# Optimization experiments

Hardware: AMD Instinct MI355X
Metric: run time of the kernel (lower is better)

The kernel has to match this reference:

```python
import jax, jax.numpy as jnp
import numpy as np

DIM = 640
HEADS = 10
HEAD_DIM = DIM // HEADS
SCALE = DIM ** (-0.5)  # note: module scales by full dim**-0.5, not head_dim


def setup_inputs() -> dict:
    key = jax.random.key(0)
    ks = jax.random.split(key, 5)
    B, N = 16, 1024
    x = jax.random.normal(ks[0], (B, N, DIM), dtype=jnp.float32)
    w_qkv = jax.random.normal(ks[1], (DIM, 3 * DIM), dtype=jnp.float32) * (DIM ** -0.5)
    b_qkv = jnp.zeros((3 * DIM,), dtype=jnp.float32)
    w_out = jax.random.normal(ks[2], (DIM, DIM), dtype=jnp.float32) * (DIM ** -0.5)
    b_out = jnp.zeros((DIM,), dtype=jnp.float32)
    return {"x": x, "w_qkv": w_qkv, "b_qkv": b_qkv, "w_out": w_out, "b_out": b_out}


def reference(x, w_qkv, b_qkv, w_out, b_out):
    B, N, _ = x.shape
    qkv = x @ w_qkv + b_qkv                     # [B, N, 3*DIM]
    qkv = qkv.reshape(B, N, 3, HEADS, HEAD_DIM)
    q, k, v = qkv[:, :, 0], qkv[:, :, 1], qkv[:, :, 2]   # [B, N, H, Dh]
    # scores: QK^T scaled by dim**-0.5 (module's normfactor)
    scores = jnp.einsum('bihd,bjhd->bhij', q, k) * SCALE  # [B, H, N, N]
    attn = jax.nn.softmax(scores, axis=-1)
    out = jnp.einsum('bhij,bjhd->bihd', attn, v)          # [B, N, H, Dh]
    out = out.reshape(B, N, DIM)
    return out @ w_out + b_out
```

## Files before the change

### kernel.cpp

```cpp
#include <hip/hip_runtime.h>

#define DIM 640
#define NHEADS 10
#define HDIM 64
#define SEQ 1024
#define BATCH 16
#define MROWS (BATCH * SEQ)
#define QKVN (3 * DIM)
#define NBH (BATCH * NHEADS)

typedef float f32x4 __attribute__((ext_vector_type(4)));
typedef __bf16 bf16x8 __attribute__((ext_vector_type(8)));

#define SM_C 0.057027536f

__device__ __forceinline__ unsigned short f2b(float f) {
  union { __bf16 h; unsigned short u; } v;
  v.h = (__bf16)f;
  return v.u;
}

__device__ __forceinline__ f32x4 mfma16(bf16x8 a, bf16x8 b, f32x4 c) {
  return __builtin_amdgcn_mfma_f32_16x16x32_bf16(a, b, c, 0, 0, 0);
}

typedef __attribute__((address_space(3))) unsigned int as3_u32;
typedef const __attribute__((address_space(1))) unsigned int as1_u32;
__device__ __forceinline__ void glds16(const unsigned short* g, unsigned short* l) {
  __builtin_amdgcn_global_load_lds((as1_u32*)g, (as3_u32*)l, 16, 0, 0);
}

__global__ __launch_bounds__(256) void convert_x(
    const float* __restrict__ X, unsigned short* __restrict__ xb) {
  int i = (blockIdx.x * 256 + threadIdx.x) * 4;
  float4 v = *(const float4*)(X + i);
  ushort4 s;
  s.x = f2b(v.x); s.y = f2b(v.y); s.z = f2b(v.z); s.w = f2b(v.w);
  *(ushort4*)(xb + i) = s;
}

__global__ __launch_bounds__(256) void transpose_w(
    const float* __restrict__ W, unsigned short* __restrict__ Wt, int R, int C) {
  __shared__ int tile[32][33];
  const int tx = threadIdx.x & 31, ty = threadIdx.x >> 5;
  const int c0 = blockIdx.x * 32, r0 = blockIdx.y * 32;
#pragma unroll
  for (int i = 0; i < 4; ++i)
    tile[ty + 8 * i][tx] = f2b(W[(r0 + ty + 8 * i) * C + c0 + tx]);
  __syncthreads();
#pragma unroll
  for (int i = 0; i < 4; ++i)
    Wt[(c0 + ty + 8 * i) * R + r0 + tx] = (unsigned short)tile[tx][ty + 8 * i];
}

__global__ __launch_bounds__(256) void qkv_gemm(
    const unsigned short* __restrict__ A, const unsigned short* __restrict__ Bt,
    const float* __restrict__ bias,
    unsigned short* __restrict__ qw, unsigned short* __restrict__ kw,
    unsigned short* __restrict__ vtw) {
  __shared__ __attribute__((aligned(16))) unsigned short As[128 * 64];
  __shared__ __attribute__((aligned(16))) unsigned short Bs[128 * 64];
  const int t = threadIdx.x;
  const int lane = t & 63, w = t >> 6;
  const int quad = lane >> 4, cl = lane & 15;
  const int m0 = blockIdx.y * 128, n0 = blockIdx.x * 128;
  const int wr = (w >> 1) * 64, wc = (w & 1) * 64;

  const int r8 = lane >> 3;
  const int sw = ((lane & 7) ^ r8) * 8;
  const unsigned short* asrc = A + (size_t)(m0 + w * 32 + r8) * DIM + sw;
  const unsigned short* bsrc = Bt + (size_t)(n0 + w * 32 + r8) * DIM + sw;

  const int x = cl & 7;
  const int aoff0 = (wr + cl) * 64 + (quad ^ x) * 8;
  const int aoff1 = (wr + cl) * 64 + ((4 + quad) ^ x) * 8;
  const int boff0 = (wc + cl) * 64 + (quad ^ x) * 8;
  const int boff1 = (wc + cl) * 64 + ((4 + quad) ^ x) * 8;

  f32x4 acc[4][4];
#pragma unroll
  for (int i = 0; i < 4; ++i)
#pragma unroll
    for (int j = 0; j < 4; ++j) acc[i][j] = (f32x4){0.f, 0.f, 0.f, 0.f};

  for (int kt = 0; kt < DIM / 64; ++kt) {
    __syncthreads();
#pragma unroll
    for (int i = 0; i < 4; ++i) {
      glds16(asrc + (size_t)i * 8 * DIM, &As[(w * 32 + i * 8) * 64]);
      glds16(bsrc + (size_t)i * 8 * DIM, &Bs[(w * 32 + i * 8) * 64]);
    }
    asrc += 64; bsrc += 64;
    __syncthreads();
#pragma unroll
    for (int ks = 0; ks < 2; ++ks) {
      const int ao = ks ? aoff1 : aoff0, bo = ks ? boff1 : boff0;
      bf16x8 af[4], bfr[4];
#pragma unroll
      for (int i = 0; i < 4; ++i) af[i] = *(const bf16x8*)&As[ao + i * 1024];
#pragma unroll
      for (int j = 0; j < 4; ++j) bfr[j] = *(const bf16x8*)&Bs[bo + j * 1024];
#pragma unroll
      for (int i = 0; i < 4; ++i)
#pragma unroll
        for (int j = 0; j < 4; ++j) acc[i][j] = mfma16(af[i], bfr[j], acc[i][j]);
    }
  }

  const int sec = n0 / DIM;
  unsigned short* qk = (sec == 0) ? qw : kw;
  const float sc = (sec == 0) ? SM_C : 1.0f;
#pragma unroll
  for (int j = 0; j < 4; ++j) {
    int cc = n0 + wc + j * 16 + cl;
    int cr = cc - sec * DIM;
    int h = cr >> 6, d = cr & 63;
    float bv = bias[cc];
#pragma unroll
    for (int i = 0; i < 4; ++i) {
      int rbase = m0 + wr + i * 16 + quad * 4;
      int b = rbase >> 10, n = rbase & 1023;
      int bh = b * NHEADS + h;
      if (sec < 2) {
        size_t base = ((size_t)bh * SEQ + n) * HDIM + d;
#pragma unroll
        for (int r = 0; r < 4; ++r)
          qk[base + (size_t)r * HDIM] = f2b((acc[i][j][r] + bv) * sc);
      } else {
        ushort4 s;
        s.x = f2b(acc[i][j][0] + bv);
        s.y = f2b(acc[i][j][1] + bv);
        s.z = f2b(acc[i][j][2] + bv);
        s.w = f2b(acc[i][j][3] + bv);
        *(ushort4*)(vtw + ((size_t)bh * HDIM + d) * SEQ + n) = s;
      }
    }
  }
}

__global__ __launch_bounds__(256) void attn_kernel(
    const unsigned short* __restrict__ qw, const unsigned short* __restrict__ kw,
    const unsigned short* __restrict__ vtw, unsigned short* __restrict__ out) {
  __shared__ __attribute__((aligned(16))) unsigned short Ks[2][64 * 64];
  __shared__ __attribute__((aligned(16))) unsigned short Vs[2][64 * 64];
  __shared__ __attribute__((aligned(16))) __bf16 Ps[4][32][72];
  const int t = threadIdx.x;
  const int lane = t & 63, w = t >> 6;
  const int quad = lane >> 4, cl = lane & 15;
  const int flat = blockIdx.x;
  const int bh = flat % NBH;
  const int qb = flat / NBH;
  const size_t qkbase = (size_t)bh * SEQ * HDIM;
  const size_t vbase  = (size_t)bh * HDIM * SEQ;

  const int r8 = lane >> 3;
  const int sw = ((lane & 7) ^ r8) * 8;
  const unsigned short* ksrc = kw + qkbase + (size_t)(w * 16 + r8) * HDIM + sw;
  const unsigned short* vsrc = vtw + vbase + (size_t)(w * 16 + r8) * SEQ + sw;

  const int x = cl & 7;
  const int koff0 = cl * 64 + (quad ^ x) * 8;
  const int koff1 = cl * 64 + ((4 + quad) ^ x) * 8;

  bf16x8 aq[2][2];
#pragma unroll
  for (int i = 0; i < 2; ++i) {
    const unsigned short* qp =
        qw + qkbase + (size_t)(qb * 128 + w * 32 + i * 16 + cl) * HDIM;
    aq[i][0] = *(const bf16x8*)(qp + quad * 8);
    aq[i][1] = *(const bf16x8*)(qp + 32 + quad * 8);
  }

  const __bf16 one = (__bf16)1.0f;
  const bf16x8 ones = {one, one, one, one, one, one, one, one};

  f32x4 o_acc[2][4];
#pragma unroll
  for (int i = 0; i < 2; ++i)
#pragma unroll
    for (int dt = 0; dt < 4; ++dt) o_acc[i][dt] = (f32x4){0.f, 0.f, 0.f, 0.f};
  f32x4 o1[2];
  o1[0] = (f32x4){0.f, 0.f, 0.f, 0.f};
  o1[1] = (f32x4){0.f, 0.f, 0.f, 0.f};

  glds16(ksrc,            &Ks[0][(w * 16) * 64]);
  glds16(ksrc + 8 * HDIM, &Ks[0][(w * 16 + 8) * 64]);
  glds16(vsrc,            &Vs[0][(w * 16) * 64]);
  glds16(vsrc + 8 * SEQ,  &Vs[0][(w * 16 + 8) * 64]);

  for (int kt = 0; kt < 16; ++kt) {
    const int cur = kt & 1, nxt = cur ^ 1;
    __syncthreads();

    const int kn = (kt + 1) & 15;
    const unsigned short* kp = ksrc + (size_t)kn * 64 * HDIM;
    const unsigned short* vp = vsrc + kn * 64;
    glds16(kp,            &Ks[nxt][(w * 16) * 64]);
    glds16(kp + 8 * HDIM, &Ks[nxt][(w * 16 + 8) * 64]);
    glds16(vp,            &Vs[nxt][(w * 16) * 64]);
    glds16(vp + 8 * SEQ,  &Vs[nxt][(w * 16 + 8) * 64]);

    const unsigned short* Kc = &Ks[cur][0];
    const unsigned short* Vc = &Vs[cur][0];

#pragma unroll
    for (int jj = 0; jj < 4; ++jj) {
      bf16x8 bk0 = *(const bf16x8*)&Kc[koff0 + jj * 1024];
      bf16x8 bk1 = *(const bf16x8*)&Kc[koff1 + jj * 1024];
#pragma unroll
      for (int i = 0; i < 2; ++i) {
        f32x4 z = (f32x4){0.f, 0.f, 0.f, 0.f};
        z = mfma16(aq[i][0], bk0, z);
        z = mfma16(aq[i][1], bk1, z);
#pragma unroll
        for (int r = 0; r < 4; ++r)
          Ps[w][i * 16 + quad * 4 + r][jj * 16 + cl] =
              (__bf16)__builtin_amdgcn_exp2f(z[r]);
      }
    }

    bf16x8 ap[2][2];
#pragma unroll
    for (int i = 0; i < 2; ++i) {
      ap[i][0] = *(const bf16x8*)&Ps[w][i * 16 + cl][quad * 8];
      ap[i][1] = *(const bf16x8*)&Ps[w][i * 16 + cl][32 + quad * 8];
    }

#pragma unroll
    for (int i = 0; i < 2; ++i) {
      o1[i] = mfma16(ap[i][0], ones, o1[i]);
      o1[i] = mfma16(ap[i][1], ones, o1[i]);
    }

#pragma unroll
    for (int dt = 0; dt < 4; ++dt) {
      bf16x8 bv0 = *(const bf16x8*)&Vc[koff0 + dt * 1024];
      bf16x8 bv1 = *(const bf16x8*)&Vc[koff1 + dt * 1024];
#pragma unroll
      for (int i = 0; i < 2; ++i) {
        o_acc[i][dt] = mfma16(ap[i][0], bv0, o_acc[i][dt]);
        o_acc[i][dt] = mfma16(ap[i][1], bv1, o_acc[i][dt]);
      }
    }
  }

  const int b = bh / NHEADS, h = bh % NHEADS;
#pragma unroll
  for (int i = 0; i < 2; ++i)
#pragma unroll
    for (int r = 0; r < 4; ++r) {
      float inv = 1.f / o1[i][r];
      int row = b * SEQ + qb * 128 + w * 32 + i * 16 + quad * 4 + r;
#pragma unroll
      for (int dt = 0; dt < 4; ++dt)
        out[(size_t)row * DIM + h * HDIM + dt * 16 + cl] =
            f2b(o_acc[i][dt][r] * inv);
    }
}

__global__ __launch_bounds__(256) void out_gemm(
    const unsigned short* __restrict__ A, const unsigned short* __restrict__ Bt,
    const float* __restrict__ bias, float* __restrict__ C) {
  __shared__ __attribute__((aligned(16))) unsigned short As[128 * 64];
  __shared__ __attribute__((aligned(16))) unsigned short Bs[128 * 64];
  const int t = threadIdx.x;
  const int lane = t & 63, w = t >> 6;
  const int quad = lane >> 4, cl = lane & 15;
  const int m0 = blockIdx.y * 128, n0 = blockIdx.x * 128;
  const int wr = (w >> 1) * 64, wc = (w & 1) * 64;

  const int r8 = lane >> 3;
  const int sw = ((lane & 7) ^ r8) * 8;
  const unsigned short* asrc = A + (size_t)(m0 + w * 32 + r8) * DIM + sw;
  const unsigned short* bsrc = Bt + (size_t)(n0 + w * 32 + r8) * DIM + sw;

  const int x = cl & 7;
  const int aoff0 = (wr + cl) * 64 + (quad ^ x) * 8;
  const int aoff1 = (wr + cl) * 64 + ((4 + quad) ^ x) * 8;
  const int boff0 = (wc + cl) * 64 + (quad ^ x) * 8;
  const int boff1 = (wc + cl) * 64 + ((4 + quad) ^ x) * 8;

  f32x4 acc[4][4];
#pragma unroll
  for (int i = 0; i < 4; ++i)
#pragma unroll
    for (int j = 0; j < 4; ++j) acc[i][j] = (f32x4){0.f, 0.f, 0.f, 0.f};

  for (int kt = 0; kt < DIM / 64; ++kt) {
    __syncthreads();
#pragma unroll
    for (int i = 0; i < 4; ++i) {
      glds16(asrc + (size_t)i * 8 * DIM, &As[(w * 32 + i * 8) * 64]);
      glds16(bsrc + (size_t)i * 8 * DIM, &Bs[(w * 32 + i * 8) * 64]);
    }
    asrc += 64; bsrc += 64;
    __syncthreads();
#pragma unroll
    for (int ks = 0; ks < 2; ++ks) {
      const int ao = ks ? aoff1 : aoff0, bo = ks ? boff1 : boff0;
      bf16x8 af[4], bfr[4];
#pragma unroll
      for (int i = 0; i < 4; ++i) af[i] = *(const bf16x8*)&As[ao + i * 1024];
#pragma unroll
      for (int j = 0; j < 4; ++j) bfr[j] = *(const bf16x8*)&Bs[bo + j * 1024];
#pragma unroll
      for (int i = 0; i < 4; ++i)
#pragma unroll
        for (int j = 0; j < 4; ++j) acc[i][j] = mfma16(af[i], bfr[j], acc[i][j]);
    }
  }
#pragma unroll
  for (int j = 0; j < 4; ++j) {
    int cc = n0 + wc + j * 16 + cl;
    float bv = bias[cc];
#pragma unroll
    for (int i = 0; i < 4; ++i) {
#pragma unroll
      for (int r = 0; r < 4; ++r) {
        int rr = m0 + wr + i * 16 + quad * 4 + r;
        C[(size_t)rr * DIM + cc] = acc[i][j][r] + bv;
      }
    }
  }
}

extern "C" void kernel_launch(void* const* d_in, const int* in_sizes, int n_in,
                              void* d_out, int out_size, void* d_ws, size_t ws_size,
                              hipStream_t stream) {
  const float* x     = (const float*)d_in[0];
  const float* w_qkv = (const float*)d_in[1];
  const float* b_qkv = (const float*)d_in[2];
  const float* w_out = (const float*)d_in[3];
  const float* b_out = (const float*)d_in[4];
  float* out = (float*)d_out;

  unsigned short* ws = (unsigned short*)d_ws;
  unsigned short* xb      = ws;
  unsigned short* wt_qkv  = ws + 10485760;
  unsigned short* wt_out  = wt_qkv + 1228800;
  unsigned short* qw      = wt_out + 409600;
  unsigned short* kw      = qw + 10485760;
  unsigned short* vtw     = kw + 10485760;
  unsigned short* attn_ws = xb;

  convert_x<<<MROWS * DIM / 1024, 256, 0, stream>>>(x, xb);
  transpose_w<<<dim3(QKVN / 32, DIM / 32), 256, 0, stream>>>(w_qkv, wt_qkv, DIM, QKVN);
  transpose_w<<<dim3(DIM / 32, DIM / 32), 256, 0, stream>>>(w_out, wt_out, DIM, DIM);
  qkv_gemm<<<dim3(QKVN / 128, MROWS / 128), 256, 0, stream>>>(xb, wt_qkv, b_qkv, qw, kw, vtw);
  attn_kernel<<<dim3(NBH * (SEQ / 128)), 256, 0, stream>>>(qw, kw, vtw, attn_ws);
  out_gemm<<<dim3(DIM / 128, MROWS / 128), 256, 0, stream>>>(attn_ws, wt_out, b_out, out);
}
```

Measured before the change: 262.6 us.

## Keep softmax probabilities in registers via transposed QK^T and 16x16x16 MFMA

Swaps the operands of the QK^T MFMA so each lane's output matches the A-operand layout of the 16x16x16 bf16 MFMA. Exponentiated scores then feed the PV and row-sum MFMAs straight from registers instead of going through the per-wave LDS P buffer. This removes the LDS writes, reads and shared memory for P, at the cost of twice as many, smaller MFMA instructions and narrower V reads from LDS. It also skips the redundant prefetch on the last iteration.

After: 256.7 us. -2.2%, faster.

```diff
diff --git a/kernel.cpp b/kernel.cpp
--- a/kernel.cpp
+++ b/kernel.cpp
@@ -11,6 +11,7 @@
 
 typedef float f32x4 __attribute__((ext_vector_type(4)));
 typedef __bf16 bf16x8 __attribute__((ext_vector_type(8)));
+typedef short s16x4 __attribute__((ext_vector_type(4)));
 
 #define SM_C 0.057027536f
 
@@ -22,6 +23,9 @@
 
 __device__ __forceinline__ f32x4 mfma16(bf16x8 a, bf16x8 b, f32x4 c) {
   return __builtin_amdgcn_mfma_f32_16x16x32_bf16(a, b, c, 0, 0, 0);
+}
+__device__ __forceinline__ f32x4 mfma1k(s16x4 a, s16x4 b, f32x4 c) {
+  return __builtin_amdgcn_mfma_f32_16x16x16bf16_1k(a, b, c, 0, 0, 0);
 }
 
 typedef __attribute__((address_space(3))) unsigned int as3_u32;
@@ -143,7 +147,6 @@
     const unsigned short* __restrict__ vtw, unsigned short* __restrict__ out) {
   __shared__ __attribute__((aligned(16))) unsigned short Ks[2][64 * 64];
   __shared__ __attribute__((aligned(16))) unsigned short Vs[2][64 * 64];
-  __shared__ __attribute__((aligned(16))) __bf16 Ps[4][32][72];
   const int t = threadIdx.x;
   const int lane = t & 63, w = t >> 6;
   const int quad = lane >> 4, cl = lane & 15;
@@ -171,8 +174,7 @@
     aq[i][1] = *(const bf16x8*)(qp + 32 + quad * 8);
   }
 
-  const __bf16 one = (__bf16)1.0f;
-  const bf16x8 ones = {one, one, one, one, one, one, one, one};
+  const s16x4 ones4 = {0x3F80, 0x3F80, 0x3F80, 0x3F80};
 
   f32x4 o_acc[2][4];
 #pragma unroll
@@ -192,17 +194,19 @@
     const int cur = kt & 1, nxt = cur ^ 1;
     __syncthreads();
 
-    const int kn = (kt + 1) & 15;
-    const unsigned short* kp = ksrc + (size_t)kn * 64 * HDIM;
-    const unsigned short* vp = vsrc + kn * 64;
-    glds16(kp,            &Ks[nxt][(w * 16) * 64]);
-    glds16(kp + 8 * HDIM, &Ks[nxt][(w * 16 + 8) * 64]);
-    glds16(vp,            &Vs[nxt][(w * 16) * 64]);
-    glds16(vp + 8 * SEQ,  &Vs[nxt][(w * 16 + 8) * 64]);
+    if (kt < 15) {
+      const unsigned short* kp = ksrc + (size_t)(kt + 1) * 64 * HDIM;
+      const unsigned short* vp = vsrc + (kt + 1) * 64;
+      glds16(kp,            &Ks[nxt][(w * 16) * 64]);
+      glds16(kp + 8 * HDIM, &Ks[nxt][(w * 16 + 8) * 64]);
+      glds16(vp,            &Vs[nxt][(w * 16) * 64]);
+      glds16(vp + 8 * SEQ,  &Vs[nxt][(w * 16 + 8) * 64]);
+    }
 
     const unsigned short* Kc = &Ks[cur][0];
     const unsigned short* Vc = &Vs[cur][0];
 
+    s16x4 pf[2][4];
 #pragma unroll
     for (int jj = 0; jj < 4; ++jj) {
       bf16x8 bk0 = *(const bf16x8*)&Kc[koff0 + jj * 1024];
@@ -210,36 +214,29 @@
 #pragma unroll
       for (int i = 0; i < 2; ++i) {
         f32x4 z = (f32x4){0.f, 0.f, 0.f, 0.f};
-        z = mfma16(aq[i][0], bk0, z);
-        z = mfma16(aq[i][1], bk1, z);
+        z = mfma16(bk0, aq[i][0], z);
+        z = mfma16(bk1, aq[i][1], z);
+        s16x4 p;
 #pragma unroll
         for (int r = 0; r < 4; ++r)
-          Ps[w][i * 16 + quad * 4 + r][jj * 16 + cl] =
-              (__bf16)__builtin_amdgcn_exp2f(z[r]);
+          p[r] = (short)f2b(__builtin_amdgcn_exp2f(z[r]));
+        pf[i][jj] = p;
+        o1[i] = mfma1k(p, ones4, o1[i]);
       }
     }
 
-    bf16x8 ap[2][2];
-#pragma unroll
-    for (int i = 0; i < 2; ++i) {
-      ap[i][0] = *(const bf16x8*)&Ps[w][i * 16 + cl][quad * 8];
-      ap[i][1] = *(const bf16x8*)&Ps[w][i * 16 + cl][32 + quad * 8];
-    }
-
-#pragma unroll
-    for (int i = 0; i < 2; ++i) {
-      o1[i] = mfma16(ap[i][0], ones, o1[i]);
-      o1[i] = mfma16(ap[i][1], ones, o1[i]);
-    }
-
 #pragma unroll
     for (int dt = 0; dt < 4; ++dt) {
-      bf16x8 bv0 = *(const bf16x8*)&Vc[koff0 + dt * 1024];
-      bf16x8 bv1 = *(const bf16x8*)&Vc[koff1 + dt * 1024];
-#pragma unroll
-      for (int i = 0; i < 2; ++i) {
-        o_acc[i][dt] = mfma16(ap[i][0], bv0, o_acc[i][dt]);
-        o_acc[i][dt] = mfma16(ap[i][1], bv1, o_acc[i][dt]);
+      const int vrow = dt * 16 + cl;
+      const int vbase_off = vrow * 64 + (quad & 1) * 4;
+      const int vxor = vrow & 7;
+#pragma unroll
+      for (int jj = 0; jj < 4; ++jj) {
+        s16x4 bv = *(const s16x4*)
+            &Vc[vbase_off + ((2 * jj + (quad >> 1)) ^ vxor) * 8];
+#pragma unroll
+        for (int i = 0; i < 2; ++i)
+          o_acc[i][dt] = mfma1k(pf[i][jj], bv, o_acc[i][dt]);
       }
     }
   }
```
